# Kernel tuning notes

Hardware: AMD Instinct MI355X
Metric: run time of the kernel (lower is better)

Reference implementation:

```python
import jax, jax.numpy as jnp
import numpy as np

NUM_HEADS = 8
NUM_GROUPS = 32
EMB = 512
EPS = 1e-5


def setup_inputs() -> dict:
    key = jax.random.key(0)
    ks = jax.random.split(key, 12)
    B, C, H, W = 256, EMB, 16, 16
    s = 1.0 / np.sqrt(C)
    x = jax.random.normal(ks[0], (B, C, H, W), dtype=jnp.float32)
    Wq = jax.random.normal(ks[1], (C, EMB), dtype=jnp.float32) * s
    bq = jax.random.normal(ks[2], (EMB,), dtype=jnp.float32) * 0.01
    Wk = jax.random.normal(ks[3], (C, EMB), dtype=jnp.float32) * s
    bk = jax.random.normal(ks[4], (EMB,), dtype=jnp.float32) * 0.01
    Wv = jax.random.normal(ks[5], (C, EMB), dtype=jnp.float32) * s
    bv = jax.random.normal(ks[6], (EMB,), dtype=jnp.float32) * 0.01
    Wf = jax.random.normal(ks[7], (EMB, EMB), dtype=jnp.float32) * s
    bf = jax.random.normal(ks[8], (EMB,), dtype=jnp.float32) * 0.01
    gn_w = jnp.ones((EMB,), dtype=jnp.float32)
    gn_b = jnp.zeros((EMB,), dtype=jnp.float32)
    return {"x": x, "Wq": Wq, "bq": bq, "Wk": Wk, "bk": bk,
            "Wv": Wv, "bv": bv, "Wf": Wf, "bf": bf,
            "gn_w": gn_w, "gn_b": gn_b}


def reference(x, Wq, bq, Wk, bk, Wv, bv, Wf, bf, gn_w, gn_b):
    B, C, H, W = x.shape
    S = H * W
    nh = NUM_HEADS
    dh = EMB // nh
    xs = x.reshape(B, C, S).transpose(0, 2, 1)  # [B, S, C]
    q = (xs @ Wq + bq).reshape(B, S, nh, dh)
    k = (xs @ Wk + bk).reshape(B, S, nh, dh)
    v = (xs @ Wv + bv).reshape(B, S, nh, dh)
    scale = dh ** -0.5
    logits = jnp.einsum('bshd,bthd->bhst', q, k) * scale  # [B, nh, S, S]
    attn = jax.nn.softmax(logits, axis=-1)
    o = jnp.einsum('bhst,bthd->bshd', attn, v).reshape(B, S, EMB)
    o = o @ Wf + bf  # [B, S, EMB]
    y = o.transpose(0, 2, 1).reshape(B, EMB, H, W) + x  # residual
    # GroupNorm over (channels-within-group, H, W)
    G = NUM_GROUPS
    yg = y.reshape(B, G, EMB // G, H, W)
    mu = jnp.mean(yg, axis=(2, 3, 4), keepdims=True)
    var = jnp.var(yg, axis=(2, 3, 4), keepdims=True)
    yn = ((yg - mu) * jax.lax.rsqrt(var + EPS)).reshape(B, EMB, H, W)
    return yn * gn_w.reshape(1, EMB, 1, 1) + gn_b.reshape(1, EMB, 1, 1)
```

## Files before the change

### kernel.cpp

```cpp
#include <hip/hip_runtime.h>
#include <hip/hip_bf16.h>
#include <stdint.h>

#define B_  256
#define C_  512
#define S_  256
#define NH  8
#define DH  64

typedef float f32x4 __attribute__((ext_vector_type(4)));
typedef short s16x8 __attribute__((ext_vector_type(8)));

static __device__ __forceinline__ unsigned short f2bf(float f) {
  union { float f; unsigned u; } v; v.f = f;
  unsigned r = v.u + 0x7FFFu + ((v.u >> 16) & 1u);
  return (unsigned short)(r >> 16);
}

static __device__ __forceinline__ unsigned pk_bf16(float lo, float hi) {
  unsigned r;
  asm("v_cvt_pk_bf16_f32 %0, %1, %2" : "=v"(r) : "v"(lo), "v"(hi));
  return r;
}

static __device__ __forceinline__ void gload_lds16(const void* g, void* l) {
  __builtin_amdgcn_global_load_lds((const __attribute__((address_space(1))) void*)g,
                                   (__attribute__((address_space(3))) void*)l,
                                   16, 0, 0);
}

__global__ __launch_bounds__(256) void prep_w(const float* __restrict__ Wq,
                                              const float* __restrict__ Wk,
                                              const float* __restrict__ Wv,
                                              const float* __restrict__ Wf,
                                              unsigned short* __restrict__ Wqkvt,
                                              unsigned short* __restrict__ Wft) {
  int mat = blockIdx.z;
  const float* src = (mat == 0) ? Wq : (mat == 1) ? Wk : (mat == 2) ? Wv : Wf;
  unsigned short* dst = (mat < 3) ? (Wqkvt + (size_t)mat * 512 * 512) : Wft;
  int n0 = blockIdx.x * 64, c0 = blockIdx.y * 64;
  __shared__ float tile[64][65];
  int t = threadIdx.x;
  int tr = t >> 4;
  int tc = (t & 15) * 4;
#pragma unroll
  for (int i = 0; i < 4; ++i) {
    int c = tr + i * 16;
    float4 v = *(const float4*)&src[(size_t)(c0 + c) * 512 + n0 + tc];
    tile[c][tc + 0] = v.x; tile[c][tc + 1] = v.y;
    tile[c][tc + 2] = v.z; tile[c][tc + 3] = v.w;
  }
  __syncthreads();
#pragma unroll
  for (int i = 0; i < 4; ++i) {
    int n = tr + i * 16;
    ushort4 o;
    o.x = f2bf(tile[tc + 0][n]); o.y = f2bf(tile[tc + 1][n]);
    o.z = f2bf(tile[tc + 2][n]); o.w = f2bf(tile[tc + 3][n]);
    *(ushort4*)&dst[(size_t)(n0 + n) * 512 + c0 + tc] = o;
  }
}

__global__ __launch_bounds__(256) void prep_x(const float* __restrict__ x,
                                              unsigned short* __restrict__ xs) {
  int b = blockIdx.z, s0 = blockIdx.x * 64, c0 = blockIdx.y * 64;
  __shared__ float tile[64][65];
  int t = threadIdx.x;
  int tr = t >> 4, tc = (t & 15) * 4;
  const float* xb = x + (size_t)b * C_ * S_;
#pragma unroll
  for (int i = 0; i < 4; ++i) {
    int c = tr + i * 16;
    float4 v = *(const float4*)&xb[(size_t)(c0 + c) * S_ + s0 + tc];
    tile[c][tc + 0] = v.x; tile[c][tc + 1] = v.y;
    tile[c][tc + 2] = v.z; tile[c][tc + 3] = v.w;
  }
  __syncthreads();
  unsigned short* xsb = xs + (size_t)b * S_ * C_;
#pragma unroll
  for (int i = 0; i < 4; ++i) {
    int s = tr + i * 16;
    ushort4 o;
    o.x = f2bf(tile[tc + 0][s]); o.y = f2bf(tile[tc + 1][s]);
    o.z = f2bf(tile[tc + 2][s]); o.w = f2bf(tile[tc + 3][s]);
    *(ushort4*)&xsb[(size_t)(s0 + s) * C_ + c0 + tc] = o;
  }
}

__global__ __launch_bounds__(256) void qkv_gemm(const unsigned short* __restrict__ xs,
                                                const unsigned short* __restrict__ Wqkvt,
                                                const float* __restrict__ bq,
                                                const float* __restrict__ bk,
                                                const float* __restrict__ bv,
                                                unsigned short* __restrict__ qout,
                                                unsigned short* __restrict__ kout,
                                                unsigned short* __restrict__ vout) {
  __shared__ char lds[49152];
  int bid = blockIdx.x;
  int lin = (bid & 7) * 768 + (bid >> 3);
  int b = lin / 24, r24 = lin % 24;
  int mt = r24 / 12, nt = r24 % 12;
  int t = threadIdx.x, lane = t & 63, w = t >> 6;
  int l15 = lane & 15, l4 = lane >> 4;
  int wr = w >> 1, wc = w & 1;
  const unsigned short* xsb = xs + ((size_t)b * S_ + mt * 128) * C_;
  const unsigned short* wt  = Wqkvt + (size_t)nt * 128 * C_;

#define QSTAGE(kt, p)                                                         \
  {                                                                           \
    _Pragma("unroll")                                                         \
    for (int i = 0; i < 2; ++i) {                                             \
      int ch = i * 256 + t, r = ch >> 2, g = ch & 3;                          \
      int gs = g ^ ((r ^ (r >> 2)) & 3);                                      \
      gload_lds16(xsb + (size_t)r * C_ + (kt) * 32 + gs * 8,                  \
                  lds + (p) * 16384 + ch * 16);                               \
    }                                                                         \
    _Pragma("unroll")                                                         \
    for (int i = 0; i < 2; ++i) {                                             \
      int ch = i * 256 + t, r = ch >> 2, g = ch & 3;                          \
      int gs = g ^ ((r ^ (r >> 2)) & 3);                                      \
      gload_lds16(wt + (size_t)r * C_ + (kt) * 32 + gs * 8,                   \
                  lds + (p) * 16384 + 8192 + ch * 16);                        \
    }                                                                         \
  }

  f32x4 acc[4][4] = {};
  QSTAGE(0, 0);
  QSTAGE(1, 1);

  int cur = 0, stg = 2;
  for (int kt = 0; kt < 16; ++kt) {
    if (kt < 15) asm volatile("s_waitcnt vmcnt(4)" ::: "memory");
    else         asm volatile("s_waitcnt vmcnt(0)" ::: "memory");
    __builtin_amdgcn_s_barrier();
    asm volatile("" ::: "memory");
    if (kt + 2 < 16) QSTAGE(kt + 2, stg);

    const char* Ab = lds + cur * 16384;
    const char* Bb = Ab + 8192;
    s16x8 af[4], bfr[4];
#pragma unroll
    for (int fi = 0; fi < 4; ++fi) {
      int r = wr * 64 + fi * 16 + l15;
      af[fi] = *(const s16x8*)(Ab + r * 64 + ((l4 ^ ((r ^ (r >> 2)) & 3)) << 4));
    }
#pragma unroll
    for (int fj = 0; fj < 4; ++fj) {
      int r = wc * 64 + fj * 16 + l15;
      bfr[fj] = *(const s16x8*)(Bb + r * 64 + ((l4 ^ ((r ^ (r >> 2)) & 3)) << 4));
    }
    __builtin_amdgcn_s_setprio(1);
#pragma unroll
    for (int fi = 0; fi < 4; ++fi)
#pragma unroll
      for (int fj = 0; fj < 4; ++fj)
        acc[fi][fj] = __builtin_amdgcn_mfma_f32_16x16x32_bf16(af[fi], bfr[fj], acc[fi][fj], 0, 0, 0);
    __builtin_amdgcn_s_setprio(0);
    cur = (cur == 2) ? 0 : cur + 1;
    stg = (stg == 2) ? 0 : stg + 1;
  }
#undef QSTAGE

  int s_base = mt * 128 + wr * 64;
#pragma unroll
  for (int fj = 0; fj < 4; ++fj) {
    int n_glob = nt * 128 + wc * 64 + fj * 16;
    int sel = n_glob >> 9;
    int within = n_glob & 511;
    int h = within >> 6, dbase = within & 63;
    const float* bias = (sel == 0) ? bq : (sel == 1) ? bk : bv;
    float bias_v = bias[within + l15];
    int d = dbase + l15;
    if (sel == 2) {
      unsigned short* vt = vout + (((size_t)b * NH + h) * DH + d) * (size_t)S_;
#pragma unroll
      for (int fi = 0; fi < 4; ++fi) {
        int srow = s_base + fi * 16 + l4 * 4;
        ushort4 o4;
        o4.x = f2bf(acc[fi][fj][0] + bias_v);
        o4.y = f2bf(acc[fi][fj][1] + bias_v);
        o4.z = f2bf(acc[fi][fj][2] + bias_v);
        o4.w = f2bf(acc[fi][fj][3] + bias_v);
        *(ushort4*)&vt[srow] = o4;
      }
    } else {
      unsigned short* dst = (sel == 0) ? qout : kout;
      unsigned short* dhead = dst + ((size_t)b * NH + h) * S_ * DH;
#pragma unroll
      for (int fi = 0; fi < 4; ++fi) {
        int srow = s_base + fi * 16 + l4 * 4;
#pragma unroll
        for (int rg = 0; rg < 4; ++rg)
          dhead[(size_t)(srow + rg) * DH + d] = f2bf(acc[fi][fj][rg] + bias_v);
      }
    }
  }
}

__global__ __launch_bounds__(512) void attn(const unsigned short* __restrict__ q,
                                            const unsigned short* __restrict__ k,
                                            const unsigned short* __restrict__ vt,
                                            unsigned short* __restrict__ o) {
  int h = blockIdx.x, b = blockIdx.y;
  const unsigned short* qh  = q  + ((size_t)b * NH + h) * S_ * DH;
  const unsigned short* kh  = k  + ((size_t)b * NH + h) * S_ * DH;
  const unsigned short* vth = vt + ((size_t)b * NH + h) * DH * S_;
  __shared__ unsigned short Ks[256 * 72];
  __shared__ unsigned short Vs[64 * 264];
  int t = threadIdx.x, lane = t & 63, w = t >> 6;
  int l15 = lane & 15, l4 = lane >> 4;

  s16x8 qf[2][2];
#pragma unroll
  for (int fi = 0; fi < 2; ++fi)
#pragma unroll
    for (int kk = 0; kk < 2; ++kk) {
      int row = w * 32 + fi * 16 + l15;
      qf[fi][kk] = *(const s16x8*)&qh[(size_t)row * DH + kk * 32 + l4 * 8];
    }

#pragma unroll
  for (int i = 0; i < 4; ++i) {
    int ch = i * 512 + t;
    int r = ch >> 3, g = ch & 7;
    int r64 = r & 63, w32 = r64 & 31;
    int rho = (r & 192) + (r64 >> 5) * 32 + ((w32 >> 2) & 1) * 16 + (w32 >> 3) * 4 + (w32 & 3);
    uint4 kv = *(const uint4*)(kh + (size_t)r * DH + g * 8);
    *(uint4*)((char*)Ks + rho * 144 + g * 16) = kv;
  }
#pragma unroll
  for (int i = 0; i < 4; ++i) {
    int ch = i * 512 + t;
    int d = ch >> 5, c32 = ch & 31;
    uint4 vv = *(const uint4*)(vth + (size_t)d * S_ + c32 * 8);
    *(uint4*)((char*)Vs + d * 528 + c32 * 16) = vv;
  }
  __syncthreads();

  f32x4 acco[4][2] = {};
  float m_run[2] = {-3e38f, -3e38f}, l_run[2] = {0.f, 0.f};
  const float SCL = 0.125f * 1.44269504089f;

  for (int kb = 0; kb < 4; ++kb) {
    f32x4 accs[4][2] = {};
#pragma unroll
    for (int kk = 0; kk < 2; ++kk) {
      s16x8 kf[4];
#pragma unroll
      for (int fj = 0; fj < 4; ++fj)
        kf[fj] = *(const s16x8*)((const char*)Ks + (kb * 64 + fj * 16 + l15) * 144 + kk * 64 + l4 * 16);
      __builtin_amdgcn_s_setprio(1);
#pragma unroll
      for (int fj = 0; fj < 4; ++fj)
#pragma unroll
        for (int fi = 0; fi < 2; ++fi)
          accs[fj][fi] = __builtin_amdgcn_mfma_f32_16x16x32_bf16(kf[fj], qf[fi][kk], accs[fj][fi], 0, 0, 0);
      __builtin_amdgcn_s_setprio(0);
    }
#pragma unroll
    for (int fi = 0; fi < 2; ++fi) {
      float mx = accs[0][fi][0];
#pragma unroll
      for (int fj = 0; fj < 4; ++fj)
#pragma unroll
        for (int rg = 0; rg < 4; ++rg) mx = fmaxf(mx, accs[fj][fi][rg]);
      mx = fmaxf(mx, __shfl_xor(mx, 16, 64));
      mx = fmaxf(mx, __shfl_xor(mx, 32, 64));
      float mnew = fmaxf(m_run[fi], mx);
      float alpha = __builtin_amdgcn_exp2f((m_run[fi] - mnew) * SCL);
      m_run[fi] = mnew;
      float lsum = 0.f;
#pragma unroll
      for (int fj = 0; fj < 4; ++fj)
#pragma unroll
        for (int rg = 0; rg < 4; ++rg) {
          float p = __builtin_amdgcn_exp2f((accs[fj][fi][rg] - mnew) * SCL);
          accs[fj][fi][rg] = p;
          lsum += p;
        }
      lsum += __shfl_xor(lsum, 16, 64);
      lsum += __shfl_xor(lsum, 32, 64);
      l_run[fi] = l_run[fi] * alpha + lsum;
#pragma unroll
      for (int fd = 0; fd < 4; ++fd)
#pragma unroll
        for (int rg = 0; rg < 4; ++rg) acco[fd][fi][rg] *= alpha;
    }
#pragma unroll
    for (int kk2 = 0; kk2 < 2; ++kk2) {
      s16x8 vf[4];
#pragma unroll
      for (int fd = 0; fd < 4; ++fd)
        vf[fd] = *(const s16x8*)((const char*)Vs + (fd * 16 + l15) * 528 + kb * 128 + kk2 * 64 + l4 * 16);
#pragma unroll
      for (int fi = 0; fi < 2; ++fi) {
        union { unsigned u[4]; s16x8 v; } pb;
        pb.u[0] = pk_bf16(accs[2 * kk2][fi][0],     accs[2 * kk2][fi][1]);
        pb.u[1] = pk_bf16(accs[2 * kk2][fi][2],     accs[2 * kk2][fi][3]);
        pb.u[2] = pk_bf16(accs[2 * kk2 + 1][fi][0], accs[2 * kk2 + 1][fi][1]);
        pb.u[3] = pk_bf16(accs[2 * kk2 + 1][fi][2], accs[2 * kk2 + 1][fi][3]);
        __builtin_amdgcn_s_setprio(1);
#pragma unroll
        for (int fd = 0; fd < 4; ++fd)
          acco[fd][fi] = __builtin_amdgcn_mfma_f32_16x16x32_bf16(vf[fd], pb.v, acco[fd][fi], 0, 0, 0);
        __builtin_amdgcn_s_setprio(0);
      }
    }
  }

  unsigned short* ob = o + (size_t)b * S_ * C_ + h * DH;
#pragma unroll
  for (int fi = 0; fi < 2; ++fi) {
    float inv = 1.0f / l_run[fi];
    int qrow = w * 32 + fi * 16 + l15;
#pragma unroll
    for (int fd = 0; fd < 4; ++fd) {
      ushort4 s4;
      s4.x = f2bf(acco[fd][fi][0] * inv);
      s4.y = f2bf(acco[fd][fi][1] * inv);
      s4.z = f2bf(acco[fd][fi][2] * inv);
      s4.w = f2bf(acco[fd][fi][3] * inv);
      *(ushort4*)&ob[(size_t)qrow * C_ + fd * 16 + l4 * 4] = s4;
    }
  }
}

__global__ __launch_bounds__(512) void proj_gn(const unsigned short* __restrict__ o,
                                               const unsigned short* __restrict__ Wft,
                                               const float* __restrict__ bfp,
                                               const float* __restrict__ x,
                                               const float* __restrict__ gnw,
                                               const float* __restrict__ gnb,
                                               float* __restrict__ out) {
  __shared__ char plds[73728];
  __shared__ float red_s[128], red_q[128];
  __shared__ float mu_s[8], rs_s[8];
  int b = blockIdx.y, ct = blockIdx.x;
  int t = threadIdx.x, lane = t & 63, w = t >> 6;
  int l15 = lane & 15, l4 = lane >> 4;
  int wc = w >> 2, wsq = w & 3;
  if (t < 128) { red_s[t] = 0.f; red_q[t] = 0.f; }
  f32x4 acc[4][4] = {};
  const unsigned short* wt = Wft + (size_t)ct * 128 * C_;
  const unsigned short* ob = o + (size_t)b * S_ * C_;

#define PSTAGE(kt, p)                                                         \
  {                                                                           \
    {                                                                         \
      int ch = t, r = ch >> 2, g = ch & 3;                                    \
      int gs = g ^ ((r ^ (r >> 2)) & 3);                                      \
      gload_lds16(wt + (size_t)r * C_ + (kt) * 32 + gs * 8,                   \
                  plds + (p) * 24576 + ch * 16);                              \
    }                                                                         \
    _Pragma("unroll")                                                         \
    for (int i = 0; i < 2; ++i) {                                             \
      int ch = i * 512 + t, r = ch >> 2, g = ch & 3;                          \
      int gs = g ^ ((r ^ (r >> 2)) & 3);                                      \
      gload_lds16(ob + (size_t)r * C_ + (kt) * 32 + gs * 8,                   \
                  plds + (p) * 24576 + 8192 + ch * 16);                       \
    }                                                                         \
  }

  PSTAGE(0, 0);
  PSTAGE(1, 1);

  int cur = 0, stg = 2;
  for (int kt = 0; kt < 16; ++kt) {
    if (kt < 15) asm volatile("s_waitcnt vmcnt(3)" ::: "memory");
    else         asm volatile("s_waitcnt vmcnt(0)" ::: "memory");
    __builtin_amdgcn_s_barrier();
    asm volatile("" ::: "memory");
    if (kt + 2 < 16) PSTAGE(kt + 2, stg);

    const char* Ab = plds + cur * 24576;
    const char* Bb = Ab + 8192;
    s16x8 af[4], bfr[4];
#pragma unroll
    for (int fi = 0; fi < 4; ++fi) {
      int r = wc * 64 + fi * 16 + l15;
      af[fi] = *(const s16x8*)(Ab + r * 64 + ((l4 ^ ((r ^ (r >> 2)) & 3)) << 4));
    }
#pragma unroll
    for (int fj = 0; fj < 4; ++fj) {
      int r = wsq * 64 + fj * 16 + l15;
      bfr[fj] = *(const s16x8*)(Bb + r * 64 + ((l4 ^ ((r ^ (r >> 2)) & 3)) << 4));
    }
    __builtin_amdgcn_s_setprio(1);
#pragma unroll
    for (int fi = 0; fi < 4; ++fi)
#pragma unroll
      for (int fj = 0; fj < 4; ++fj)
        acc[fi][fj] = __builtin_amdgcn_mfma_f32_16x16x32_bf16(af[fi], bfr[fj], acc[fi][fj], 0, 0, 0);
    __builtin_amdgcn_s_setprio(0);
    cur = (cur == 2) ? 0 : cur + 1;
    stg = (stg == 2) ? 0 : stg + 1;
  }
#undef PSTAGE

  const float* xb = x + (size_t)b * C_ * S_;
  int c_base = ct * 128 + wc * 64;
  int s_base = wsq * 64;
#pragma unroll
  for (int fi = 0; fi < 4; ++fi)
#pragma unroll
    for (int rg = 0; rg < 4; ++rg) {
      int c = c_base + fi * 16 + l4 * 4 + rg;
      float bias_v = bfp[c];
      float psum = 0.f, psq = 0.f;
#pragma unroll
      for (int fj = 0; fj < 4; ++fj) {
        int s = s_base + fj * 16 + l15;
        float y = acc[fi][fj][rg] + bias_v + xb[(size_t)c * S_ + s];
        acc[fi][fj][rg] = y;
        psum += y; psq += y * y;
      }
#pragma unroll
      for (int off = 1; off < 16; off <<= 1) {
        psum += __shfl_xor(psum, off, 64);
        psq += __shfl_xor(psq, off, 64);
      }
      if (l15 == 0) {
        int cl = c - ct * 128;
        atomicAdd(&red_s[cl], psum);
        atomicAdd(&red_q[cl], psq);
      }
    }
  __syncthreads();
  if (t < 8) {
    float s = 0.f, qq = 0.f;
#pragma unroll
    for (int i = 0; i < 16; ++i) { s += red_s[t * 16 + i]; qq += red_q[t * 16 + i]; }
    float mu = s * (1.0f / 4096.0f);
    float var = qq * (1.0f / 4096.0f) - mu * mu;
    mu_s[t] = mu;
    rs_s[t] = rsqrtf(var + 1e-5f);
  }
  __syncthreads();
  float* outb = out + (size_t)b * C_ * S_;
#pragma unroll
  for (int fi = 0; fi < 4; ++fi)
#pragma unroll
    for (int rg = 0; rg < 4; ++rg) {
      int c = c_base + fi * 16 + l4 * 4 + rg;
      int gl = (c - ct * 128) >> 4;
      float mu = mu_s[gl], rs = rs_s[gl];
      float gw = gnw[c], gb = gnb[c];
#pragma unroll
      for (int fj = 0; fj < 4; ++fj) {
        int s = s_base + fj * 16 + l15;
        outb[(size_t)c * S_ + s] = (acc[fi][fj][rg] - mu) * rs * gw + gb;
      }
    }
}

extern "C" void kernel_launch(void* const* d_in, const int* in_sizes, int n_in,
                              void* d_out, int out_size, void* d_ws, size_t ws_size,
                              hipStream_t stream) {
  const float* x   = (const float*)d_in[0];
  const float* Wq  = (const float*)d_in[1];
  const float* bq  = (const float*)d_in[2];
  const float* Wk  = (const float*)d_in[3];
  const float* bk  = (const float*)d_in[4];
  const float* Wv  = (const float*)d_in[5];
  const float* bv  = (const float*)d_in[6];
  const float* Wf  = (const float*)d_in[7];
  const float* bf  = (const float*)d_in[8];
  const float* gnw = (const float*)d_in[9];
  const float* gnb = (const float*)d_in[10];

  char* ws = (char*)d_ws;
  unsigned short* Wqkvt = (unsigned short*)ws;
  unsigned short* Wft   = (unsigned short*)(ws + 0x180000);
  unsigned short* xs    = (unsigned short*)(ws + 0x200000);
  unsigned short* vbuf  = (unsigned short*)(ws + 0x200000 + (size_t)B_ * S_ * C_ * 2);
  unsigned short* qbuf  = (unsigned short*)d_out;
  unsigned short* kbuf  = qbuf + (size_t)B_ * NH * S_ * DH;
  unsigned short* obuf  = xs;
  float* out = (float*)d_out;

  hipLaunchKernelGGL(prep_w, dim3(8, 8, 4), dim3(256), 0, stream, Wq, Wk, Wv, Wf, Wqkvt, Wft);
  hipLaunchKernelGGL(prep_x, dim3(4, 8, 256), dim3(256), 0, stream, x, xs);
  hipLaunchKernelGGL(qkv_gemm, dim3(6144), dim3(256), 0, stream,
                     xs, Wqkvt, bq, bk, bv, qbuf, kbuf, vbuf);
  hipLaunchKernelGGL(attn, dim3(8, 256), dim3(512), 0, stream, qbuf, kbuf, vbuf, obuf);
  hipLaunchKernelGGL(proj_gn, dim3(4, 256), dim3(512), 0, stream,
                     obuf, Wft, bf, x, gnw, gnb, out);
}
```

Measured before the change: 379.9 us.

## Enlarge QKV GEMM tile to 256x256 with 8 waves and split-phase loads

The QKV projection GEMM moves from 128x128 tiles with 4 waves to 256x256 tiles with 8 waves. Each wave now computes 128x64, with 32 accumulators instead of 16. The LDS pipeline grows to 4 stages of 32 KB using a simpler swizzle. Each k-step is split into two halves with an extra barrier, so the next A tile loads during the first MFMA half and the next B tile during the second. The aim is more data reuse per loaded byte and fewer global loads, at the cost of 128 KB LDS per block (one block per CU) and higher register pressure.

```diff
diff --git a/kernel.cpp b/kernel.cpp
--- a/kernel.cpp
+++ b/kernel.cpp
@@ -87,7 +87,7 @@
   }
 }
 
-__global__ __launch_bounds__(256) void qkv_gemm(const unsigned short* __restrict__ xs,
+__global__ __launch_bounds__(512) void qkv_gemm(const unsigned short* __restrict__ xs,
                                                 const unsigned short* __restrict__ Wqkvt,
                                                 const float* __restrict__ bq,
                                                 const float* __restrict__ bk,
@@ -95,76 +95,93 @@
                                                 unsigned short* __restrict__ qout,
                                                 unsigned short* __restrict__ kout,
                                                 unsigned short* __restrict__ vout) {
-  __shared__ char lds[49152];
+  __shared__ char lds[131072];
   int bid = blockIdx.x;
-  int lin = (bid & 7) * 768 + (bid >> 3);
-  int b = lin / 24, r24 = lin % 24;
-  int mt = r24 / 12, nt = r24 % 12;
+  int lin = (bid & 7) * 192 + (bid >> 3);
+  int b = lin / 6, nt = lin % 6;
   int t = threadIdx.x, lane = t & 63, w = t >> 6;
   int l15 = lane & 15, l4 = lane >> 4;
-  int wr = w >> 1, wc = w & 1;
-  const unsigned short* xsb = xs + ((size_t)b * S_ + mt * 128) * C_;
-  const unsigned short* wt  = Wqkvt + (size_t)nt * 128 * C_;
-
-#define QSTAGE(kt, p)                                                         \
+  int wr = w >> 2, wc = w & 3;
+  const unsigned short* xsb = xs + (size_t)b * S_ * C_;
+  const unsigned short* wt  = Wqkvt + (size_t)nt * 256 * C_;
+
+#define STAGE_A(kt, p)                                                        \
   {                                                                           \
     _Pragma("unroll")                                                         \
     for (int i = 0; i < 2; ++i) {                                             \
-      int ch = i * 256 + t, r = ch >> 2, g = ch & 3;                          \
-      int gs = g ^ ((r ^ (r >> 2)) & 3);                                      \
+      int ch = i * 512 + t, r = ch >> 2, g = ch & 3;                          \
+      int gs = g ^ ((r >> 1) & 3);                                            \
       gload_lds16(xsb + (size_t)r * C_ + (kt) * 32 + gs * 8,                  \
-                  lds + (p) * 16384 + ch * 16);                               \
+                  lds + (p) * 32768 + ch * 16);                               \
     }                                                                         \
+  }
+#define STAGE_B(kt, p)                                                        \
+  {                                                                           \
     _Pragma("unroll")                                                         \
     for (int i = 0; i < 2; ++i) {                                             \
-      int ch = i * 256 + t, r = ch >> 2, g = ch & 3;                          \
-      int gs = g ^ ((r ^ (r >> 2)) & 3);                                      \
+      int ch = i * 512 + t, r = ch >> 2, g = ch & 3;                          \
+      int gs = g ^ ((r >> 1) & 3);                                            \
       gload_lds16(wt + (size_t)r * C_ + (kt) * 32 + gs * 8,                   \
-                  lds + (p) * 16384 + 8192 + ch * 16);                        \
+                  lds + (p) * 32768 + 16384 + ch * 16);                       \
     }                                                                         \
   }
 
-  f32x4 acc[4][4] = {};
-  QSTAGE(0, 0);
-  QSTAGE(1, 1);
-
-  int cur = 0, stg = 2;
+  f32x4 acc[8][4] = {};
+  STAGE_A(0, 0); STAGE_B(0, 0);
+  STAGE_A(1, 1); STAGE_B(1, 1);
+
   for (int kt = 0; kt < 16; ++kt) {
     if (kt < 15) asm volatile("s_waitcnt vmcnt(4)" ::: "memory");
     else         asm volatile("s_waitcnt vmcnt(0)" ::: "memory");
     __builtin_amdgcn_s_barrier();
     asm volatile("" ::: "memory");
-    if (kt + 2 < 16) QSTAGE(kt + 2, stg);
-
-    const char* Ab = lds + cur * 16384;
-    const char* Bb = Ab + 8192;
-    s16x8 af[4], bfr[4];
+
+    const char* Ab = lds + (kt & 3) * 32768;
+    const char* Bb = Ab + 16384;
+
+    s16x8 alo[4], bfr[4];
 #pragma unroll
     for (int fi = 0; fi < 4; ++fi) {
-      int r = wr * 64 + fi * 16 + l15;
-      af[fi] = *(const s16x8*)(Ab + r * 64 + ((l4 ^ ((r ^ (r >> 2)) & 3)) << 4));
+      int r = wr * 128 + fi * 16 + l15;
+      alo[fi] = *(const s16x8*)(Ab + r * 64 + ((l4 ^ ((r >> 1) & 3)) << 4));
     }
 #pragma unroll
     for (int fj = 0; fj < 4; ++fj) {
       int r = wc * 64 + fj * 16 + l15;
-      bfr[fj] = *(const s16x8*)(Bb + r * 64 + ((l4 ^ ((r ^ (r >> 2)) & 3)) << 4));
-    }
+      bfr[fj] = *(const s16x8*)(Bb + r * 64 + ((l4 ^ ((r >> 1) & 3)) << 4));
+    }
+    if (kt + 2 < 16) STAGE_A(kt + 2, (kt + 2) & 3);
     __builtin_amdgcn_s_setprio(1);
 #pragma unroll
     for (int fi = 0; fi < 4; ++fi)
 #pragma unroll
       for (int fj = 0; fj < 4; ++fj)
-        acc[fi][fj] = __builtin_amdgcn_mfma_f32_16x16x32_bf16(af[fi], bfr[fj], acc[fi][fj], 0, 0, 0);
+        acc[fi][fj] = __builtin_amdgcn_mfma_f32_16x16x32_bf16(alo[fi], bfr[fj], acc[fi][fj], 0, 0, 0);
     __builtin_amdgcn_s_setprio(0);
-    cur = (cur == 2) ? 0 : cur + 1;
-    stg = (stg == 2) ? 0 : stg + 1;
-  }
-#undef QSTAGE
-
-  int s_base = mt * 128 + wr * 64;
+    __builtin_amdgcn_s_barrier();
+
+    s16x8 ahi[4];
+#pragma unroll
+    for (int fi = 0; fi < 4; ++fi) {
+      int r = wr * 128 + 64 + fi * 16 + l15;
+      ahi[fi] = *(const s16x8*)(Ab + r * 64 + ((l4 ^ ((r >> 1) & 3)) << 4));
+    }
+    if (kt + 2 < 16) STAGE_B(kt + 2, (kt + 2) & 3);
+    __builtin_amdgcn_s_setprio(1);
+#pragma unroll
+    for (int fi = 0; fi < 4; ++fi)
+#pragma unroll
+      for (int fj = 0; fj < 4; ++fj)
+        acc[4 + fi][fj] = __builtin_amdgcn_mfma_f32_16x16x32_bf16(ahi[fi], bfr[fj], acc[4 + fi][fj], 0, 0, 0);
+    __builtin_amdgcn_s_setprio(0);
+  }
+#undef STAGE_A
+#undef STAGE_B
+
+  int s_base = wr * 128;
 #pragma unroll
   for (int fj = 0; fj < 4; ++fj) {
-    int n_glob = nt * 128 + wc * 64 + fj * 16;
+    int n_glob = nt * 256 + wc * 64 + fj * 16;
     int sel = n_glob >> 9;
     int within = n_glob & 511;
     int h = within >> 6, dbase = within & 63;
@@ -174,7 +191,7 @@
     if (sel == 2) {
       unsigned short* vt = vout + (((size_t)b * NH + h) * DH + d) * (size_t)S_;
 #pragma unroll
-      for (int fi = 0; fi < 4; ++fi) {
+      for (int fi = 0; fi < 8; ++fi) {
         int srow = s_base + fi * 16 + l4 * 4;
         ushort4 o4;
         o4.x = f2bf(acc[fi][fj][0] + bias_v);
@@ -187,7 +204,7 @@
       unsigned short* dst = (sel == 0) ? qout : kout;
       unsigned short* dhead = dst + ((size_t)b * NH + h) * S_ * DH;
 #pragma unroll
-      for (int fi = 0; fi < 4; ++fi) {
+      for (int fi = 0; fi < 8; ++fi) {
         int srow = s_base + fi * 16 + l4 * 4;
 #pragma unroll
         for (int rg = 0; rg < 4; ++rg)
@@ -480,7 +497,7 @@
 
   hipLaunchKernelGGL(prep_w, dim3(8, 8, 4), dim3(256), 0, stream, Wq, Wk, Wv, Wf, Wqkvt, Wft);
   hipLaunchKernelGGL(prep_x, dim3(4, 8, 256), dim3(256), 0, stream, x, xs);
-  hipLaunchKernelGGL(qkv_gemm, dim3(6144), dim3(256), 0, stream,
+  hipLaunchKernelGGL(qkv_gemm, dim3(1536), dim3(512), 0, stream,
                      xs, Wqkvt, bq, bk, bv, qbuf, kbuf, vbuf);
   hipLaunchKernelGGL(attn, dim3(8, 256), dim3(512), 0, stream, qbuf, kbuf, vbuf, obuf);
   hipLaunchKernelGGL(proj_gn, dim3(4, 256), dim3(512), 0, stream,
```

New measurement: 373.6 us. No clear change (-1.6%).

## Fuse QKV projection into attention kernel per batch-head, keep Q/K/V in LDS

Applied to the files above, without the earlier changes.

Merges the QKV GEMM and attention kernels into one kernel where each block computes the 256x192 Q/K/V tile for one (batch, head) from xs and head-packed weights. The results are written directly into LDS in the layouts attention expects, avoiding the global round trip of Q/K/V. The weight prep is changed to a per-head packed layout. The proj_gn loop also reorders its prefetch and barriers so LDS fragment loads happen before the next stage is issued. The cost is about 112KB of LDS per block, which limits occupancy. Each head's block also rereads the full x tile for its batch, so xs is reloaded 8 times.

```diff
diff --git a/kernel.cpp b/kernel.cpp
--- a/kernel.cpp
+++ b/kernel.cpp
@@ -33,11 +33,10 @@
                                               const float* __restrict__ Wk,
                                               const float* __restrict__ Wv,
                                               const float* __restrict__ Wf,
-                                              unsigned short* __restrict__ Wqkvt,
+                                              unsigned short* __restrict__ Whead,
                                               unsigned short* __restrict__ Wft) {
   int mat = blockIdx.z;
   const float* src = (mat == 0) ? Wq : (mat == 1) ? Wk : (mat == 2) ? Wv : Wf;
-  unsigned short* dst = (mat < 3) ? (Wqkvt + (size_t)mat * 512 * 512) : Wft;
   int n0 = blockIdx.x * 64, c0 = blockIdx.y * 64;
   __shared__ float tile[64][65];
   int t = threadIdx.x;
@@ -51,13 +50,16 @@
     tile[c][tc + 2] = v.z; tile[c][tc + 3] = v.w;
   }
   __syncthreads();
+  int h = n0 >> 6;
+  unsigned short* dst = (mat < 3) ? (Whead + ((size_t)h * 192 + mat * 64) * 512)
+                                  : (Wft + (size_t)n0 * 512);
 #pragma unroll
   for (int i = 0; i < 4; ++i) {
-    int n = tr + i * 16;
+    int nl = tr + i * 16;
     ushort4 o;
-    o.x = f2bf(tile[tc + 0][n]); o.y = f2bf(tile[tc + 1][n]);
-    o.z = f2bf(tile[tc + 2][n]); o.w = f2bf(tile[tc + 3][n]);
-    *(ushort4*)&dst[(size_t)(n0 + n) * 512 + c0 + tc] = o;
+    o.x = f2bf(tile[tc + 0][nl]); o.y = f2bf(tile[tc + 1][nl]);
+    o.z = f2bf(tile[tc + 2][nl]); o.w = f2bf(tile[tc + 3][nl]);
+    *(ushort4*)&dst[(size_t)nl * 512 + c0 + tc] = o;
   }
 }
 
@@ -87,128 +89,114 @@
   }
 }
 
-__global__ __launch_bounds__(256) void qkv_gemm(const unsigned short* __restrict__ xs,
-                                                const unsigned short* __restrict__ Wqkvt,
-                                                const float* __restrict__ bq,
-                                                const float* __restrict__ bk,
-                                                const float* __restrict__ bv,
-                                                unsigned short* __restrict__ qout,
-                                                unsigned short* __restrict__ kout,
-                                                unsigned short* __restrict__ vout) {
-  __shared__ char lds[49152];
+__global__ __launch_bounds__(512) void qkvattn(const unsigned short* __restrict__ xs,
+                                               const unsigned short* __restrict__ Whead,
+                                               const float* __restrict__ bq,
+                                               const float* __restrict__ bk,
+                                               const float* __restrict__ bv,
+                                               unsigned short* __restrict__ o) {
+  __shared__ __align__(16) char lds[114688];
   int bid = blockIdx.x;
-  int lin = (bid & 7) * 768 + (bid >> 3);
-  int b = lin / 24, r24 = lin % 24;
-  int mt = r24 / 12, nt = r24 % 12;
+  int lin = (bid & 7) * 256 + (bid >> 3);
+  int h = lin & 7, b = lin >> 3;
   int t = threadIdx.x, lane = t & 63, w = t >> 6;
   int l15 = lane & 15, l4 = lane >> 4;
-  int wr = w >> 1, wc = w & 1;
-  const unsigned short* xsb = xs + ((size_t)b * S_ + mt * 128) * C_;
-  const unsigned short* wt  = Wqkvt + (size_t)nt * 128 * C_;
-
-#define QSTAGE(kt, p)                                                         \
+  int wr = w >> 2, wc = w & 3;
+  const unsigned short* xsb = xs + (size_t)b * S_ * C_;
+  const unsigned short* wh  = Whead + (size_t)h * 192 * C_;
+
+#define FSTAGE(kt, p)                                                         \
   {                                                                           \
     _Pragma("unroll")                                                         \
-    for (int i = 0; i < 2; ++i) {                                             \
-      int ch = i * 256 + t, r = ch >> 2, g = ch & 3;                          \
-      int gs = g ^ ((r ^ (r >> 2)) & 3);                                      \
-      gload_lds16(xsb + (size_t)r * C_ + (kt) * 32 + gs * 8,                  \
-                  lds + (p) * 16384 + ch * 16);                               \
+    for (int i = 0; i < 4; ++i) {                                             \
+      int ch = i * 512 + t, r = ch >> 3, g = ch & 7;                          \
+      int gs = g ^ (r & 7);                                                   \
+      gload_lds16(xsb + (size_t)r * C_ + (kt) * 64 + gs * 8,                  \
+                  lds + (p) * 57344 + ch * 16);                               \
     }                                                                         \
     _Pragma("unroll")                                                         \
-    for (int i = 0; i < 2; ++i) {                                             \
-      int ch = i * 256 + t, r = ch >> 2, g = ch & 3;                          \
-      int gs = g ^ ((r ^ (r >> 2)) & 3);                                      \
-      gload_lds16(wt + (size_t)r * C_ + (kt) * 32 + gs * 8,                   \
-                  lds + (p) * 16384 + 8192 + ch * 16);                        \
+    for (int i = 0; i < 3; ++i) {                                             \
+      int ch = i * 512 + t, r = ch >> 3, g = ch & 7;                          \
+      int gs = g ^ (r & 7);                                                   \
+      gload_lds16(wh + (size_t)r * C_ + (kt) * 64 + gs * 8,                   \
+                  lds + (p) * 57344 + 32768 + ch * 16);                       \
     }                                                                         \
   }
 
-  f32x4 acc[4][4] = {};
-  QSTAGE(0, 0);
-  QSTAGE(1, 1);
-
-  int cur = 0, stg = 2;
-  for (int kt = 0; kt < 16; ++kt) {
-    if (kt < 15) asm volatile("s_waitcnt vmcnt(4)" ::: "memory");
-    else         asm volatile("s_waitcnt vmcnt(0)" ::: "memory");
+  f32x4 acc[8][3] = {};
+  FSTAGE(0, 0);
+
+  for (int kt = 0; kt < 8; ++kt) {
+    if (kt < 7) FSTAGE(kt + 1, (kt + 1) & 1);
+    if (kt < 7) asm volatile("s_waitcnt vmcnt(7)" ::: "memory");
+    else        asm volatile("s_waitcnt vmcnt(0)" ::: "memory");
     __builtin_amdgcn_s_barrier();
     asm volatile("" ::: "memory");
-    if (kt + 2 < 16) QSTAGE(kt + 2, stg);
-
-    const char* Ab = lds + cur * 16384;
-    const char* Bb = Ab + 8192;
-    s16x8 af[4], bfr[4];
-#pragma unroll
-    for (int fi = 0; fi < 4; ++fi) {
-      int r = wr * 64 + fi * 16 + l15;
-      af[fi] = *(const s16x8*)(Ab + r * 64 + ((l4 ^ ((r ^ (r >> 2)) & 3)) << 4));
-    }
-#pragma unroll
-    for (int fj = 0; fj < 4; ++fj) {
-      int r = wc * 64 + fj * 16 + l15;
-      bfr[fj] = *(const s16x8*)(Bb + r * 64 + ((l4 ^ ((r ^ (r >> 2)) & 3)) << 4));
-    }
-    __builtin_amdgcn_s_setprio(1);
-#pragma unroll
-    for (int fi = 0; fi < 4; ++fi)
-#pragma unroll
-      for (int fj = 0; fj < 4; ++fj)
-        acc[fi][fj] = __builtin_amdgcn_mfma_f32_16x16x32_bf16(af[fi], bfr[fj], acc[fi][fj], 0, 0, 0);
-    __builtin_amdgcn_s_setprio(0);
-    cur = (cur == 2) ? 0 : cur + 1;
-    stg = (stg == 2) ? 0 : stg + 1;
-  }
-#undef QSTAGE
-
-  int s_base = mt * 128 + wr * 64;
-#pragma unroll
-  for (int fj = 0; fj < 4; ++fj) {
-    int n_glob = nt * 128 + wc * 64 + fj * 16;
-    int sel = n_glob >> 9;
-    int within = n_glob & 511;
-    int h = within >> 6, dbase = within & 63;
+    const char* Ab = lds + (kt & 1) * 57344;
+    const char* Bb = Ab + 32768;
+#pragma unroll
+    for (int kk = 0; kk < 2; ++kk) {
+      s16x8 afr[8], bfr[3];
+#pragma unroll
+      for (int fi = 0; fi < 8; ++fi) {
+        int r = wr * 128 + fi * 16 + l15;
+        afr[fi] = *(const s16x8*)(Ab + r * 128 + (((kk * 4 + l4) ^ (r & 7)) << 4));
+      }
+#pragma unroll
+      for (int fj = 0; fj < 3; ++fj) {
+        int r = wc * 48 + fj * 16 + l15;
+        bfr[fj] = *(const s16x8*)(Bb + r * 128 + (((kk * 4 + l4) ^ (r & 7)) << 4));
+      }
+      __builtin_amdgcn_s_setprio(1);
+#pragma unroll
+      for (int fi = 0; fi < 8; ++fi)
+#pragma unroll
+        for (int fj = 0; fj < 3; ++fj)
+          acc[fi][fj] = __builtin_amdgcn_mfma_f32_16x16x32_bf16(afr[fi], bfr[fj], acc[fi][fj], 0, 0, 0);
+      __builtin_amdgcn_s_setprio(0);
+    }
+    __builtin_amdgcn_s_barrier();
+  }
+#undef FSTAGE
+
+  unsigned short* Ql = (unsigned short*)lds;
+  unsigned short* Kl = (unsigned short*)(lds + 36864);
+  unsigned short* Vl = (unsigned short*)(lds + 73728);
+  int h64 = h * 64;
+#pragma unroll
+  for (int fj = 0; fj < 3; ++fj) {
+    int n = wc * 48 + fj * 16 + l15;
+    int sel = n >> 6, d = n & 63;
     const float* bias = (sel == 0) ? bq : (sel == 1) ? bk : bv;
-    float bias_v = bias[within + l15];
-    int d = dbase + l15;
+    float bias_v = bias[h64 + d];
     if (sel == 2) {
-      unsigned short* vt = vout + (((size_t)b * NH + h) * DH + d) * (size_t)S_;
-#pragma unroll
-      for (int fi = 0; fi < 4; ++fi) {
-        int srow = s_base + fi * 16 + l4 * 4;
+#pragma unroll
+      for (int fi = 0; fi < 8; ++fi) {
+        int s0 = wr * 128 + fi * 16 + l4 * 4;
         ushort4 o4;
         o4.x = f2bf(acc[fi][fj][0] + bias_v);
         o4.y = f2bf(acc[fi][fj][1] + bias_v);
         o4.z = f2bf(acc[fi][fj][2] + bias_v);
         o4.w = f2bf(acc[fi][fj][3] + bias_v);
-        *(ushort4*)&vt[srow] = o4;
+        *(ushort4*)&Vl[d * 264 + s0] = o4;
       }
     } else {
-      unsigned short* dst = (sel == 0) ? qout : kout;
-      unsigned short* dhead = dst + ((size_t)b * NH + h) * S_ * DH;
-#pragma unroll
-      for (int fi = 0; fi < 4; ++fi) {
-        int srow = s_base + fi * 16 + l4 * 4;
-#pragma unroll
-        for (int rg = 0; rg < 4; ++rg)
-          dhead[(size_t)(srow + rg) * DH + d] = f2bf(acc[fi][fj][rg] + bias_v);
-      }
-    }
-  }
-}
-
-__global__ __launch_bounds__(512) void attn(const unsigned short* __restrict__ q,
-                                            const unsigned short* __restrict__ k,
-                                            const unsigned short* __restrict__ vt,
-                                            unsigned short* __restrict__ o) {
-  int h = blockIdx.x, b = blockIdx.y;
-  const unsigned short* qh  = q  + ((size_t)b * NH + h) * S_ * DH;
-  const unsigned short* kh  = k  + ((size_t)b * NH + h) * S_ * DH;
-  const unsigned short* vth = vt + ((size_t)b * NH + h) * DH * S_;
-  __shared__ unsigned short Ks[256 * 72];
-  __shared__ unsigned short Vs[64 * 264];
-  int t = threadIdx.x, lane = t & 63, w = t >> 6;
-  int l15 = lane & 15, l4 = lane >> 4;
+      unsigned short* dstl = (sel == 0) ? Ql : Kl;
+#pragma unroll
+      for (int fi = 0; fi < 8; ++fi)
+#pragma unroll
+        for (int rg = 0; rg < 4; ++rg) {
+          int s = wr * 128 + fi * 16 + l4 * 4 + rg;
+          int row = s;
+          if (sel == 1) {
+            int s64 = s & 63, w32 = s64 & 31;
+            row = (s & 192) + (s64 >> 5) * 32 + ((w32 >> 2) & 1) * 16 + (w32 >> 3) * 4 + (w32 & 3);
+          }
+          dstl[row * 72 + d] = f2bf(acc[fi][fj][rg] + bias_v);
+        }
+    }
+  }
+  __syncthreads();
 
   s16x8 qf[2][2];
 #pragma unroll
@@ -216,26 +204,8 @@
 #pragma unroll
     for (int kk = 0; kk < 2; ++kk) {
       int row = w * 32 + fi * 16 + l15;
-      qf[fi][kk] = *(const s16x8*)&qh[(size_t)row * DH + kk * 32 + l4 * 8];
-    }
-
-#pragma unroll
-  for (int i = 0; i < 4; ++i) {
-    int ch = i * 512 + t;
-    int r = ch >> 3, g = ch & 7;
-    int r64 = r & 63, w32 = r64 & 31;
-    int rho = (r & 192) + (r64 >> 5) * 32 + ((w32 >> 2) & 1) * 16 + (w32 >> 3) * 4 + (w32 & 3);
-    uint4 kv = *(const uint4*)(kh + (size_t)r * DH + g * 8);
-    *(uint4*)((char*)Ks + rho * 144 + g * 16) = kv;
-  }
-#pragma unroll
-  for (int i = 0; i < 4; ++i) {
-    int ch = i * 512 + t;
-    int d = ch >> 5, c32 = ch & 31;
-    uint4 vv = *(const uint4*)(vth + (size_t)d * S_ + c32 * 8);
-    *(uint4*)((char*)Vs + d * 528 + c32 * 16) = vv;
-  }
-  __syncthreads();
+      qf[fi][kk] = *(const s16x8*)((const char*)lds + row * 144 + kk * 64 + l4 * 16);
+    }
 
   f32x4 acco[4][2] = {};
   float m_run[2] = {-3e38f, -3e38f}, l_run[2] = {0.f, 0.f};
@@ -248,7 +218,7 @@
       s16x8 kf[4];
 #pragma unroll
       for (int fj = 0; fj < 4; ++fj)
-        kf[fj] = *(const s16x8*)((const char*)Ks + (kb * 64 + fj * 16 + l15) * 144 + kk * 64 + l4 * 16);
+        kf[fj] = *(const s16x8*)((const char*)lds + 36864 + (kb * 64 + fj * 16 + l15) * 144 + kk * 64 + l4 * 16);
       __builtin_amdgcn_s_setprio(1);
 #pragma unroll
       for (int fj = 0; fj < 4; ++fj)
@@ -291,7 +261,7 @@
       s16x8 vf[4];
 #pragma unroll
       for (int fd = 0; fd < 4; ++fd)
-        vf[fd] = *(const s16x8*)((const char*)Vs + (fd * 16 + l15) * 528 + kb * 128 + kk2 * 64 + l4 * 16);
+        vf[fd] = *(const s16x8*)((const char*)lds + 73728 + (fd * 16 + l15) * 528 + kb * 128 + kk2 * 64 + l4 * 16);
 #pragma unroll
       for (int fi = 0; fi < 2; ++fi) {
         union { unsigned u[4]; s16x8 v; } pb;
@@ -363,15 +333,11 @@
 
   PSTAGE(0, 0);
   PSTAGE(1, 1);
+  asm volatile("s_waitcnt vmcnt(3)" ::: "memory");
+  __builtin_amdgcn_s_barrier();
 
   int cur = 0, stg = 2;
   for (int kt = 0; kt < 16; ++kt) {
-    if (kt < 15) asm volatile("s_waitcnt vmcnt(3)" ::: "memory");
-    else         asm volatile("s_waitcnt vmcnt(0)" ::: "memory");
-    __builtin_amdgcn_s_barrier();
-    asm volatile("" ::: "memory");
-    if (kt + 2 < 16) PSTAGE(kt + 2, stg);
-
     const char* Ab = plds + cur * 24576;
     const char* Bb = Ab + 8192;
     s16x8 af[4], bfr[4];
@@ -385,6 +351,12 @@
       int r = wsq * 64 + fj * 16 + l15;
       bfr[fj] = *(const s16x8*)(Bb + r * 64 + ((l4 ^ ((r ^ (r >> 2)) & 3)) << 4));
     }
+    if (kt + 2 < 16) PSTAGE(kt + 2, stg);
+    if (kt < 14)       asm volatile("s_waitcnt vmcnt(3)" ::: "memory");
+    else if (kt == 14) asm volatile("s_waitcnt vmcnt(0)" ::: "memory");
+    __builtin_amdgcn_s_barrier();
+    asm volatile("s_waitcnt lgkmcnt(0)" ::: "memory");
+    __builtin_amdgcn_sched_barrier(0);
     __builtin_amdgcn_s_setprio(1);
 #pragma unroll
     for (int fi = 0; fi < 4; ++fi)
@@ -392,6 +364,7 @@
       for (int fj = 0; fj < 4; ++fj)
         acc[fi][fj] = __builtin_amdgcn_mfma_f32_16x16x32_bf16(af[fi], bfr[fj], acc[fi][fj], 0, 0, 0);
     __builtin_amdgcn_s_setprio(0);
+    __builtin_amdgcn_s_barrier();
     cur = (cur == 2) ? 0 : cur + 1;
     stg = (stg == 2) ? 0 : stg + 1;
   }
@@ -469,20 +442,16 @@
   const float* gnb = (const float*)d_in[10];
 
   char* ws = (char*)d_ws;
-  unsigned short* Wqkvt = (unsigned short*)ws;
+  unsigned short* Whead = (unsigned short*)ws;
   unsigned short* Wft   = (unsigned short*)(ws + 0x180000);
   unsigned short* xs    = (unsigned short*)(ws + 0x200000);
-  unsigned short* vbuf  = (unsigned short*)(ws + 0x200000 + (size_t)B_ * S_ * C_ * 2);
-  unsigned short* qbuf  = (unsigned short*)d_out;
-  unsigned short* kbuf  = qbuf + (size_t)B_ * NH * S_ * DH;
-  unsigned short* obuf  = xs;
+  unsigned short* obuf  = (unsigned short*)(ws + 0x200000 + (size_t)B_ * S_ * C_ * 2);
   float* out = (float*)d_out;
 
-  hipLaunchKernelGGL(prep_w, dim3(8, 8, 4), dim3(256), 0, stream, Wq, Wk, Wv, Wf, Wqkvt, Wft);
+  hipLaunchKernelGGL(prep_w, dim3(8, 8, 4), dim3(256), 0, stream, Wq, Wk, Wv, Wf, Whead, Wft);
   hipLaunchKernelGGL(prep_x, dim3(4, 8, 256), dim3(256), 0, stream, x, xs);
-  hipLaunchKernelGGL(qkv_gemm, dim3(6144), dim3(256), 0, stream,
-                     xs, Wqkvt, bq, bk, bv, qbuf, kbuf, vbuf);
-  hipLaunchKernelGGL(attn, dim3(8, 256), dim3(512), 0, stream, qbuf, kbuf, vbuf, obuf);
+  hipLaunchKernelGGL(qkvattn, dim3(2048), dim3(512), 0, stream,
+                     xs, Whead, bq, bk, bv, obuf);
   hipLaunchKernelGGL(proj_gn, dim3(4, 256), dim3(512), 0, stream,
                      obuf, Wft, bf, x, gnw, gnb, out);
 }
```

Measured after the change: 321.1 us. -15.5%, faster.
